# Kernel optimization log

Hardware: AMD Instinct MI355X
Metric: run time of the kernel (lower is better)

## Reference

```python
import jax, jax.numpy as jnp
import numpy as np

N = 50000      # nodes
E = 800000     # edges (avg degree 16)
D = 64         # node_feature_dim
ED = 1         # edge_feature_dim
H = 128        # hidden_dim
G = 128        # graphs in batch
L = 3          # n_conv
EPS = 1e-5     # batchnorm eps


def setup_inputs() -> dict:
    key = jax.random.key(0)
    ks = jax.random.split(key, 20)
    w = lambda k, shp: (jax.random.normal(k, shp, dtype=jnp.float32)
                        / np.float32(np.sqrt(shp[-2] if len(shp) > 1 else 1.0)))
    return {
        "atom_z": jax.random.randint(ks[0], (N,), 0, 100),
        "edge_index": jax.random.randint(ks[1], (2, E), 0, N),
        "edge_attr": jax.random.normal(ks[2], (E, ED), dtype=jnp.float32),
        "batch": jnp.sort(jax.random.randint(ks[3], (N,), 0, G)),
        "emb": jax.random.normal(ks[4], (100, D), dtype=jnp.float32),
        "edge_W1": w(ks[5], (L, 2 * D + ED, H)), "edge_b1": jnp.zeros((L, H)),
        "edge_W2": w(ks[6], (L, H, H)),          "edge_b2": jnp.zeros((L, H)),
        "node_W1": w(ks[7], (L, D + H, H)),      "node_b1": jnp.zeros((L, H)),
        "node_W2": w(ks[8], (L, H, D)),          "node_b2": jnp.zeros((L, D)),
        "bn_gamma": jnp.ones((L, D)),            "bn_beta": jnp.zeros((L, D)),
        "out_W1": w(ks[9], (D, H)),  "out_b1": jnp.zeros((H,)),
        "out_W2": w(ks[10], (H, 1)), "out_b2": jnp.zeros((1,)),
    }


def reference(atom_z, edge_index, edge_attr, batch, emb,
              edge_W1, edge_b1, edge_W2, edge_b2,
              node_W1, node_b1, node_W2, node_b2,
              bn_gamma, bn_beta, out_W1, out_b1, out_W2, out_b2):
    sp = jax.nn.softplus
    src, dst = edge_index[0], edge_index[1]  # PyG source_to_target: x_j = x[src], x_i = x[dst]
    x = emb[atom_z]                          # [N, D]
    for l in range(L):
        # --- CGConv layer l ---
        z = jnp.concatenate([x[dst], x[src], edge_attr], axis=-1)        # [E, 2D+ED]
        m = sp(sp(z @ edge_W1[l] + edge_b1[l]) @ edge_W2[l] + edge_b2[l])  # [E, H]
        aggr = jax.ops.segment_sum(m, dst, num_segments=N)               # [N, H]
        h = jnp.concatenate([x, aggr], axis=-1)                          # [N, D+H]
        x = sp(h @ node_W1[l] + node_b1[l]) @ node_W2[l] + node_b2[l] + x
        # --- BatchNorm1d (training-mode batch stats) ---
        mu = jnp.mean(x, axis=0)
        var = jnp.mean(jnp.square(x - mu), axis=0)
        x = bn_gamma[l] * (x - mu) * jax.lax.rsqrt(var + EPS) + bn_beta[l]
    # --- global mean pool over graphs ---
    sums = jax.ops.segment_sum(x, batch, num_segments=G)                 # [G, D]
    cnts = jax.ops.segment_sum(jnp.ones((N, 1), x.dtype), batch, num_segments=G)
    pooled = sums / jnp.maximum(cnts, 1.0)
    # --- output MLP (dropout is identity at eval) ---
    out = sp(pooled @ out_W1 + out_b1) @ out_W2 + out_b2                 # [G, 1]
    return out
```

## Files before the change

kernel.cpp:

```cpp
#include <hip/hip_runtime.h>
#include <hip/hip_bf16.h>

#define N_NODES 50000
#define N_EDGES 800000
#define DIM 64
#define HID 128
#define NGRAPH 128
#define BN_EPS 1e-5f

typedef __attribute__((ext_vector_type(8))) short short8;
typedef __attribute__((ext_vector_type(4))) short short4v;
typedef __attribute__((ext_vector_type(4))) float f32x4;
typedef __attribute__((ext_vector_type(4))) int int4v;

__device__ __forceinline__ float sp_(float v) {
    return fmaxf(v, 0.f) + __logf(1.f + __expf(-fabsf(v)));
}
__device__ __forceinline__ short bfb(float f) {
    __hip_bfloat16 h = __float2bfloat16(f);
    return __builtin_bit_cast(short, h);
}
__device__ __forceinline__ float b2f(short s) {
    unsigned u = ((unsigned)(unsigned short)s) << 16;
    return __builtin_bit_cast(float, u);
}

__global__ void k_embed(const int* __restrict__ az, const float* __restrict__ emb,
                        float* __restrict__ x, __hip_bfloat16* __restrict__ xb) {
    int idx = blockIdx.x * 256 + threadIdx.x;
    if (idx >= N_NODES * DIM) return;
    int n = idx >> 6;
    int d = idx & 63;
    float v = emb[az[n] * DIM + d];
    x[idx] = v;
    xb[idx] = __float2bfloat16(v);
}

__global__ void k_wprep(const float* __restrict__ src, short* __restrict__ dst,
                        int total, int nshift, int srcStride) {
    int l = blockIdx.y;
    int idx = blockIdx.x * 256 + threadIdx.x;
    if (idx >= total) return;
    int K = total >> nshift;
    int k = idx >> nshift;
    int n = idx & ((1 << nshift) - 1);
    dst[(size_t)l * total + n * K + k] = bfb(src[(size_t)l * srcStride + idx]);
}

__global__ void k_hist(const int* __restrict__ edst, int* __restrict__ deg) {
    int e = blockIdx.x * 256 + threadIdx.x;
    if (e < N_EDGES) atomicAdd(&deg[edst[e]], 1);
}

__global__ void k_scan(const int* __restrict__ deg, int* __restrict__ cursor) {
    __shared__ int wsum[16];
    __shared__ int carry;
    const int t = threadIdx.x, lane = t & 63, w = t >> 6;
    if (t == 0) carry = 0;
    __syncthreads();
    for (int base = 0; base < N_NODES; base += 1024) {
        int i = base + t;
        int v = (i < N_NODES) ? deg[i] : 0;
        int s = v;
#pragma unroll
        for (int off = 1; off < 64; off <<= 1) {
            int u = __shfl_up(s, off);
            if (lane >= off) s += u;
        }
        if (lane == 63) wsum[w] = s;
        __syncthreads();
        if (w == 0) {
            int ws = (lane < 16) ? wsum[lane] : 0;
#pragma unroll
            for (int off = 1; off < 16; off <<= 1) {
                int u = __shfl_up(ws, off);
                if (lane >= off) ws += u;
            }
            if (lane < 16) wsum[lane] = ws;
        }
        __syncthreads();
        int woff = (w == 0) ? 0 : wsum[w - 1];
        int excl = carry + woff + s - v;
        if (i < N_NODES) cursor[i] = excl;
        __syncthreads();
        if (t == 1023) carry += wsum[15];
        __syncthreads();
    }
}

__global__ void k_scatter(const int* __restrict__ esrc, const int* __restrict__ edst,
                          const float* __restrict__ eattr, int* __restrict__ cursor,
                          int* __restrict__ ssrc, int* __restrict__ sdst,
                          float* __restrict__ sattr) {
    int e = blockIdx.x * 256 + threadIdx.x;
    if (e >= N_EDGES) return;
    int d = edst[e];
    int pos = atomicAdd(&cursor[d], 1);
    ssrc[pos] = esrc[e];
    sdst[pos] = d;
    sattr[pos] = eattr[e];
}

__global__ void k_gbounds(const int* __restrict__ batch, int* __restrict__ gstart) {
    int g = threadIdx.x;
    if (g > NGRAPH) return;
    int lo = 0, hi = N_NODES;
    while (lo < hi) {
        int mid = (lo + hi) >> 1;
        if (batch[mid] < g) lo = mid + 1; else hi = mid;
    }
    gstart[g] = lo;
}

__launch_bounds__(512, 4)
__global__ void k_edge(const __hip_bfloat16* __restrict__ xb,
                       const int* __restrict__ ssrc, const int* __restrict__ sdst,
                       const float* __restrict__ sattr,
                       const float* __restrict__ W1f, const float* __restrict__ b1,
                       const float* __restrict__ b2,
                       const short* __restrict__ w1T, const short* __restrict__ w2T,
                       float* __restrict__ aggr) {
    __shared__ short zt[64 * 128];
    __shared__ short ht[64 * 128];
    __shared__ float attr_s[64];
    __shared__ int   dst_s[64];
    __shared__ int   seg_start[65];
    __shared__ int   seg_dst[64];
    __shared__ int   nseg_s;

    const int t = threadIdx.x;
    const int wid = t >> 6, lane = t & 63;
    const int lrow = lane & 15, lk = lane >> 4;
    const int r = t >> 3, q = t & 7;
    const int col = wid * 16 + lrow;

    short8 w1f[4], w2f[4];
#pragma unroll
    for (int ks = 0; ks < 4; ks++) {
        int kb = ks * 64 + lk * 16;
        w1f[ks] = *(const short8*)((const char*)w1T + col * 256 + kb);
        w2f[ks] = *(const short8*)((const char*)w2T + col * 256 + kb);
    }
    const float b1v = b1[col];
    const float b2v = b2[col];
    const float wlv = W1f[128 * 128 + col];

    const int NT = N_EDGES / 64;
    const int tile0 = blockIdx.x * 25;
    const int tile1 = (tile0 + 25 < NT) ? tile0 + 25 : NT;

    for (int tile = tile0; tile < tile1; ++tile) {
        const int e0 = tile * 64;
        {
            int e = e0 + r;
            int dn = sdst[e], sn = ssrc[e];
            if (q == 0) { dst_s[r] = dn; attr_s[r] = sattr[e]; }
            int node = (q < 4) ? dn : sn;
            const __hip_bfloat16* xr = xb + (size_t)node * DIM + (q & 3) * 16;
            int4v v0 = *(const int4v*)(xr);
            int4v v1 = *(const int4v*)(xr + 8);
            int cb = (q >> 2) * 128 + (q & 3) * 32;
            *(int4v*)((char*)zt + r * 256 + (cb ^ ((r & 7) << 4))) = v0;
            *(int4v*)((char*)zt + r * 256 + ((cb + 16) ^ ((r & 7) << 4))) = v1;
        }
        __syncthreads();

        if (wid == 0) {
            int d = dst_s[lane];
            int prev = (lane == 0) ? -1 : dst_s[lane - 1];
            bool start = (d != prev);
            unsigned long long mask = __ballot(start);
            int sidx = __popcll(mask & ((1ull << lane) - 1));
            if (start) { seg_start[sidx] = lane; seg_dst[sidx] = d; }
            if (lane == 63) {
                int ns = __popcll(mask);
                nseg_s = ns;
                seg_start[ns] = 64;
            }
        }

        f32x4 acc[4];
#pragma unroll
        for (int mi = 0; mi < 4; mi++) acc[mi] = (f32x4){0.f, 0.f, 0.f, 0.f};
#pragma unroll
        for (int ks = 0; ks < 4; ks++) {
            int kb = ks * 64 + lk * 16;
            short8 av[4];
#pragma unroll
            for (int mi = 0; mi < 4; mi++) {
                int row = mi * 16 + lrow;
                av[mi] = *(const short8*)((const char*)zt + row * 256 + (kb ^ ((row & 7) << 4)));
            }
#pragma unroll
            for (int mi = 0; mi < 4; mi++)
                acc[mi] = __builtin_amdgcn_mfma_f32_16x16x32_bf16(av[mi], w1f[ks], acc[mi], 0, 0, 0);
        }
#pragma unroll
        for (int mi = 0; mi < 4; mi++) {
#pragma unroll
            for (int rr = 0; rr < 4; rr++) {
                int row = mi * 16 + lk * 4 + rr;
                float val = acc[mi][rr] + b1v + attr_s[row] * wlv;
                *(short*)((char*)ht + row * 256 + ((col * 2) ^ ((row & 7) << 4))) = bfb(sp_(val));
            }
        }
        __syncthreads();

        f32x4 acc2[4];
#pragma unroll
        for (int mi = 0; mi < 4; mi++) acc2[mi] = (f32x4){0.f, 0.f, 0.f, 0.f};
#pragma unroll
        for (int ks = 0; ks < 4; ks++) {
            int kb = ks * 64 + lk * 16;
            short8 av[4];
#pragma unroll
            for (int mi = 0; mi < 4; mi++) {
                int row = mi * 16 + lrow;
                av[mi] = *(const short8*)((const char*)ht + row * 256 + (kb ^ ((row & 7) << 4)));
            }
#pragma unroll
            for (int mi = 0; mi < 4; mi++)
                acc2[mi] = __builtin_amdgcn_mfma_f32_16x16x32_bf16(av[mi], w2f[ks], acc2[mi], 0, 0, 0);
        }
#pragma unroll
        for (int mi = 0; mi < 4; mi++) {
#pragma unroll
            for (int rr = 0; rr < 4; rr++) {
                int row = mi * 16 + lk * 4 + rr;
                float val = sp_(acc2[mi][rr] + b2v);
                *(short*)((char*)zt + row * 256 + ((col * 2) ^ ((row & 7) << 4))) = bfb(val);
            }
        }
        __syncthreads();

        {
            int nseg = nseg_s;
            int rcol = t & 127, h = t >> 7;
            for (int s = h; s < nseg; s += 4) {
                int r0 = seg_start[s], r1 = seg_start[s + 1];
                float sum = 0.f;
                for (int rr = r0; rr < r1; rr++)
                    sum += b2f(*(const short*)((const char*)zt + rr * 256 + ((rcol * 2) ^ ((rr & 7) << 4))));
                atomicAdd(&aggr[(size_t)seg_dst[s] * HID + rcol], sum);
            }
        }
        __syncthreads();
    }
}

__launch_bounds__(256, 3)
__global__ void k_node(const __hip_bfloat16* __restrict__ xb,
                       const float* __restrict__ xf,
                       const float* __restrict__ aggr,
                       const short* __restrict__ w1T, const float* __restrict__ b1,
                       const short* __restrict__ w2T, const float* __restrict__ b2,
                       float* __restrict__ y, float* __restrict__ stats) {
    __shared__ short at[64 * 192];
    __shared__ short ht[64 * 128];

    const int t = threadIdx.x;
    const int wid = t >> 6, lane = t & 63, lrow = lane & 15, lk = lane >> 4;
    const int n0 = blockIdx.x * 64;

    const int nc0 = wid * 32;
    short8 w1f[6][2];
    float b1v[2];
#pragma unroll
    for (int ni = 0; ni < 2; ni++) {
        int col = nc0 + ni * 16 + lrow;
#pragma unroll
        for (int ks = 0; ks < 6; ks++) {
            int kb = ks * 64 + lk * 16;
            w1f[ks][ni] = *(const short8*)((const char*)w1T + col * 384 + kb);
        }
        b1v[ni] = b1[col];
    }
    const int nc2 = wid * 16;
    const int col2 = nc2 + lrow;
    short8 w2f[4];
#pragma unroll
    for (int ks = 0; ks < 4; ks++)
        w2f[ks] = *(const short8*)((const char*)w2T + col2 * 256 + ks * 64 + lk * 16);
    const float b2v = b2[col2];

    if (t < 64) {
        int node = n0 + t;
        if (node < N_NODES) {
            const __hip_bfloat16* xr = xb + (size_t)node * DIM;
#pragma unroll
            for (int i = 0; i < 8; i++) {
                int4v v = *(const int4v*)(xr + i * 8);
                *(int4v*)((char*)at + t * 384 + ((i * 16) ^ ((t & 7) << 4))) = v;
            }
        } else {
            int4v z = {0, 0, 0, 0};
#pragma unroll
            for (int i = 0; i < 8; i++)
                *(int4v*)((char*)at + t * 384 + ((i * 16) ^ ((t & 7) << 4))) = z;
        }
    }
    {
        int r = t >> 2, q = t & 3;
        int node = n0 + r;
#pragma unroll
        for (int i = 0; i < 4; i++) {
            short8 s = {0, 0, 0, 0, 0, 0, 0, 0};
            if (node < N_NODES) {
                const float* ar = aggr + (size_t)node * HID + q * 32 + i * 8;
                float4 f0 = *(const float4*)ar;
                float4 f1 = *(const float4*)(ar + 4);
                s = (short8){bfb(f0.x), bfb(f0.y), bfb(f0.z), bfb(f0.w),
                             bfb(f1.x), bfb(f1.y), bfb(f1.z), bfb(f1.w)};
            }
            int cb = 128 + q * 64 + i * 16;
            *(short8*)((char*)at + r * 384 + (cb ^ ((r & 7) << 4))) = s;
        }
    }
    __syncthreads();

    f32x4 acc[4][2];
#pragma unroll
    for (int mi = 0; mi < 4; mi++)
#pragma unroll
        for (int ni = 0; ni < 2; ni++) acc[mi][ni] = (f32x4){0.f, 0.f, 0.f, 0.f};
#pragma unroll
    for (int ks = 0; ks < 6; ks++) {
        int kb = ks * 64 + lk * 16;
        short8 av[4];
#pragma unroll
        for (int mi = 0; mi < 4; mi++) {
            int row = mi * 16 + lrow;
            av[mi] = *(const short8*)((const char*)at + row * 384 + (kb ^ ((row & 7) << 4)));
        }
#pragma unroll
        for (int mi = 0; mi < 4; mi++)
#pragma unroll
            for (int ni = 0; ni < 2; ni++)
                acc[mi][ni] = __builtin_amdgcn_mfma_f32_16x16x32_bf16(av[mi], w1f[ks][ni], acc[mi][ni], 0, 0, 0);
    }
#pragma unroll
    for (int mi = 0; mi < 4; mi++) {
#pragma unroll
        for (int ni = 0; ni < 2; ni++) {
            int col = nc0 + ni * 16 + lrow;
#pragma unroll
            for (int rr = 0; rr < 4; rr++) {
                int row = mi * 16 + lk * 4 + rr;
                float val = sp_(acc[mi][ni][rr] + b1v[ni]);
                *(short*)((char*)ht + row * 256 + ((col * 2) ^ ((row & 7) << 4))) = bfb(val);
            }
        }
    }
    __syncthreads();

    f32x4 acc2[4];
#pragma unroll
    for (int mi = 0; mi < 4; mi++) acc2[mi] = (f32x4){0.f, 0.f, 0.f, 0.f};
#pragma unroll
    for (int ks = 0; ks < 4; ks++) {
        int kb = ks * 64 + lk * 16;
        short8 av[4];
#pragma unroll
        for (int mi = 0; mi < 4; mi++) {
            int row = mi * 16 + lrow;
            av[mi] = *(const short8*)((const char*)ht + row * 256 + (kb ^ ((row & 7) << 4)));
        }
#pragma unroll
        for (int mi = 0; mi < 4; mi++)
            acc2[mi] = __builtin_amdgcn_mfma_f32_16x16x32_bf16(av[mi], w2f[ks], acc2[mi], 0, 0, 0);
    }
    float s1 = 0.f, s2 = 0.f;
#pragma unroll
    for (int mi = 0; mi < 4; mi++) {
#pragma unroll
        for (int rr = 0; rr < 4; rr++) {
            int row = mi * 16 + lk * 4 + rr;
            int node = n0 + row;
            if (node < N_NODES) {
                float v = acc2[mi][rr] + b2v + xf[(size_t)node * DIM + col2];
                y[(size_t)node * DIM + col2] = v;
                s1 += v;
                s2 += v * v;
            }
        }
    }
    s1 += __shfl_xor(s1, 16); s1 += __shfl_xor(s1, 32);
    s2 += __shfl_xor(s2, 16); s2 += __shfl_xor(s2, 32);
    if (lane < 16) {
        atomicAdd(&stats[col2], s1);
        atomicAdd(&stats[64 + col2], s2);
    }
}

__global__ void k_bnfin(const float* __restrict__ gamma, const float* __restrict__ beta,
                        float* __restrict__ stats) {
    int d = threadIdx.x;
    float mu = stats[d] * (1.f / N_NODES);
    float var = stats[64 + d] * (1.f / N_NODES) - mu * mu;
    float rstd = rsqrtf(var + BN_EPS);
    float a = gamma[d] * rstd;
    stats[128 + d] = a;
    stats[192 + d] = beta[d] - mu * a;
}

__global__ void k_bnapply(const float* __restrict__ y, const float* __restrict__ stats,
                          float* __restrict__ x, __hip_bfloat16* __restrict__ xb) {
    int idx = (blockIdx.x * 256 + threadIdx.x) * 4;
    if (idx >= N_NODES * DIM) return;
    int d = idx & 63;
    float4 v = *(const float4*)(y + idx);
    float4 r;
    r.x = stats[128 + d + 0] * v.x + stats[192 + d + 0];
    r.y = stats[128 + d + 1] * v.y + stats[192 + d + 1];
    r.z = stats[128 + d + 2] * v.z + stats[192 + d + 2];
    r.w = stats[128 + d + 3] * v.w + stats[192 + d + 3];
    *(float4*)(x + idx) = r;
    short4v s = {bfb(r.x), bfb(r.y), bfb(r.z), bfb(r.w)};
    *(short4v*)((char*)(xb + idx)) = s;
}

__global__ void k_pool2(const int* __restrict__ gstart, const float* __restrict__ x,
                        float* __restrict__ pooled) {
    __shared__ float red[256];
    const int g = blockIdx.x, t = threadIdx.x;
    const int d = t & 63, nl = t >> 6;
    const int s = gstart[g], e = gstart[g + 1];
    float sum = 0.f;
    for (int n = s + nl; n < e; n += 4)
        sum += x[(size_t)n * DIM + d];
    red[t] = sum;
    __syncthreads();
    if (t < 64) {
        float tot = red[t] + red[t + 64] + red[t + 128] + red[t + 192];
        int c = e - s;
        pooled[g * DIM + t] = tot / fmaxf((float)c, 1.f);
    }
}

__global__ void k_out(const float* __restrict__ pooled,
                      const float* __restrict__ W1, const float* __restrict__ b1,
                      const float* __restrict__ W2, const float* __restrict__ b2,
                      float* __restrict__ out) {
    __shared__ float pl[64];
    __shared__ float wsum[2];
    int g = blockIdx.x, t = threadIdx.x;
    if (t < 64) pl[t] = pooled[g * 64 + t];
    __syncthreads();
    float a = b1[t];
#pragma unroll
    for (int d = 0; d < 64; d++) a += pl[d] * W1[d * 128 + t];
    float c = sp_(a) * W2[t];
#pragma unroll
    for (int off = 32; off >= 1; off >>= 1) c += __shfl_down(c, off);
    int lane = t & 63, wid = t >> 6;
    if (lane == 0) wsum[wid] = c;
    __syncthreads();
    if (t == 0) out[g] = wsum[0] + wsum[1] + b2[0];
}

extern "C" void kernel_launch(void* const* d_in, const int* in_sizes, int n_in,
                              void* d_out, int out_size, void* d_ws, size_t ws_size,
                              hipStream_t stream) {
    const int*   az    = (const int*)d_in[0];
    const int*   ei    = (const int*)d_in[1];
    const float* eattr = (const float*)d_in[2];
    const int*   batch = (const int*)d_in[3];
    const float* emb   = (const float*)d_in[4];
    const float* eW1   = (const float*)d_in[5];
    const float* eb1   = (const float*)d_in[6];
    const float* eW2   = (const float*)d_in[7];
    const float* eb2   = (const float*)d_in[8];
    const float* nW1   = (const float*)d_in[9];
    const float* nb1   = (const float*)d_in[10];
    const float* nW2   = (const float*)d_in[11];
    const float* nb2   = (const float*)d_in[12];
    const float* gam   = (const float*)d_in[13];
    const float* bet   = (const float*)d_in[14];
    const float* oW1   = (const float*)d_in[15];
    const float* ob1   = (const float*)d_in[16];
    const float* oW2   = (const float*)d_in[17];
    const float* ob2   = (const float*)d_in[18];
    const int* esrc = ei;
    const int* edst = ei + N_EDGES;

    float* x     = (float*)d_ws;
    float* y     = x + (size_t)N_NODES * DIM;
    float* aggr  = y + (size_t)N_NODES * DIM;
    float* stats = aggr + (size_t)N_NODES * HID;
    float* pooled = stats + 256;
    __hip_bfloat16* xb = (__hip_bfloat16*)(pooled + NGRAPH * DIM);
    short* ew1T = (short*)(xb + (size_t)N_NODES * DIM);
    short* ew2T = ew1T + 3 * 128 * 128;
    short* nw1T = ew2T + 3 * 128 * 128;
    short* nw2T = nw1T + 3 * 128 * 192;
    int*   cursor = (int*)(nw2T + 3 * 64 * 128);
    int*   ssrc   = cursor + N_NODES;
    int*   sdstA  = ssrc + N_EDGES;
    float* sattr  = (float*)(sdstA + N_EDGES);
    int*   gstart = (int*)(sattr + N_EDGES);

    k_embed<<<(N_NODES * DIM + 255) / 256, 256, 0, stream>>>(az, emb, x, xb);

    k_wprep<<<dim3(64, 3), 256, 0, stream>>>(eW1, ew1T, 128 * 128, 7, 129 * 128);
    k_wprep<<<dim3(64, 3), 256, 0, stream>>>(eW2, ew2T, 128 * 128, 7, 128 * 128);
    k_wprep<<<dim3(96, 3), 256, 0, stream>>>(nW1, nw1T, 192 * 128, 7, 192 * 128);
    k_wprep<<<dim3(32, 3), 256, 0, stream>>>(nW2, nw2T, 128 * 64, 6, 128 * 64);

    hipMemsetAsync(cursor, 0, N_NODES * sizeof(int), stream);
    k_hist<<<(N_EDGES + 255) / 256, 256, 0, stream>>>(edst, cursor);
    k_scan<<<1, 1024, 0, stream>>>(cursor, cursor);
    k_scatter<<<(N_EDGES + 255) / 256, 256, 0, stream>>>(esrc, edst, eattr, cursor,
                                                         ssrc, sdstA, sattr);
    k_gbounds<<<1, 256, 0, stream>>>(batch, gstart);

    for (int l = 0; l < 3; l++) {
        hipMemsetAsync(aggr, 0, ((size_t)N_NODES * HID + 256) * sizeof(float), stream);
        k_edge<<<500, 512, 0, stream>>>(xb, ssrc, sdstA, sattr,
                                        eW1 + (size_t)l * 129 * 128, eb1 + l * 128, eb2 + l * 128,
                                        ew1T + (size_t)l * 128 * 128, ew2T + (size_t)l * 128 * 128,
                                        aggr);
        k_node<<<(N_NODES + 63) / 64, 256, 0, stream>>>(xb, x, aggr,
                                                        nw1T + (size_t)l * 128 * 192, nb1 + l * 128,
                                                        nw2T + (size_t)l * 64 * 128, nb2 + l * 64,
                                                        y, stats);
        k_bnfin<<<1, 64, 0, stream>>>(gam + l * 64, bet + l * 64, stats);
        k_bnapply<<<(N_NODES * DIM / 4 + 255) / 256, 256, 0, stream>>>(y, stats, x, xb);
    }

    k_pool2<<<NGRAPH, 256, 0, stream>>>(gstart, x, pooled);
    k_out<<<NGRAPH, 128, 0, stream>>>(pooled, oW1, ob1, oW2, ob2, (float*)d_out);
}
```

Measured before the change: 1.037 ms.

## Precompute per-node first-layer edge projections and gather them instead of raw features

The first edge-MLP matmul is split algebraically: x[dst]@W1a + x[src]@W1b is computed once per node in a new k_ab kernel, which writes a 128+128 bf16 projection per node. The edge kernel then gathers the two projections, adds them plus the edge-attribute term, and applies softplus, so one MFMA GEMM per edge tile is dropped. The message tile is also kept in fp32 in shared memory for the segment reduction. In exchange each edge gathers 512 bytes instead of 256, uses more LDS per block, and rounds the pre-activation sum to bf16.

```diff
diff --git a/kernel.cpp b/kernel.cpp
--- a/kernel.cpp
+++ b/kernel.cpp
@@ -112,17 +112,85 @@
     gstart[g] = lo;
 }
 
+__launch_bounds__(512, 2)
+__global__ void k_ab(const __hip_bfloat16* __restrict__ xb,
+                     const short* __restrict__ w1T, const float* __restrict__ b1,
+                     short* __restrict__ xab) {
+    __shared__ short xt[64 * 64];
+    __shared__ short ot[64 * 256];
+    const int t = threadIdx.x;
+    const int wid = t >> 6, lane = t & 63, lrow = lane & 15, lk = lane >> 4;
+    const int col = wid * 16 + lrow;
+    const int n0 = blockIdx.x * 64;
+
+    short8 wa[2], wb[2];
+#pragma unroll
+    for (int ks = 0; ks < 2; ks++) {
+        wa[ks] = *(const short8*)((const char*)w1T + col * 256 + ks * 64 + lk * 16);
+        wb[ks] = *(const short8*)((const char*)w1T + col * 256 + 128 + ks * 64 + lk * 16);
+    }
+    const float b1v = b1[col];
+
+    {
+        int r = t >> 3, q = t & 7;
+        int node = n0 + r;
+        int4v v = {0, 0, 0, 0};
+        if (node < N_NODES) v = *(const int4v*)(xb + (size_t)node * DIM + q * 8);
+        *(int4v*)((char*)xt + r * 128 + ((q * 16) ^ ((r & 7) << 4))) = v;
+    }
+    __syncthreads();
+
+    f32x4 aa[4], ab[4];
+#pragma unroll
+    for (int mi = 0; mi < 4; mi++) { aa[mi] = (f32x4){0.f,0.f,0.f,0.f}; ab[mi] = (f32x4){0.f,0.f,0.f,0.f}; }
+#pragma unroll
+    for (int ks = 0; ks < 2; ks++) {
+        int kb = ks * 64 + lk * 16;
+        short8 av[4];
+#pragma unroll
+        for (int mi = 0; mi < 4; mi++) {
+            int row = mi * 16 + lrow;
+            av[mi] = *(const short8*)((const char*)xt + row * 128 + (kb ^ ((row & 7) << 4)));
+        }
+#pragma unroll
+        for (int mi = 0; mi < 4; mi++) {
+            aa[mi] = __builtin_amdgcn_mfma_f32_16x16x32_bf16(av[mi], wa[ks], aa[mi], 0, 0, 0);
+            ab[mi] = __builtin_amdgcn_mfma_f32_16x16x32_bf16(av[mi], wb[ks], ab[mi], 0, 0, 0);
+        }
+    }
+#pragma unroll
+    for (int mi = 0; mi < 4; mi++) {
+#pragma unroll
+        for (int rr = 0; rr < 4; rr++) {
+            int row = mi * 16 + lk * 4 + rr;
+            int swz = (row & 7) << 4;
+            *(short*)((char*)ot + row * 512 + ((col * 2) ^ swz)) = bfb(aa[mi][rr] + b1v);
+            *(short*)((char*)ot + row * 512 + 256 + ((col * 2) ^ swz)) = bfb(ab[mi][rr]);
+        }
+    }
+    __syncthreads();
+#pragma unroll
+    for (int it = 0; it < 4; it++) {
+        int idx = it * 8192 + t * 16;
+        int row = idx >> 9, off = idx & 511;
+        int node = n0 + row;
+        if (node < N_NODES) {
+            int base = off & 256, lo = off & 255;
+            int4v v = *(const int4v*)((char*)ot + row * 512 + base + (lo ^ ((row & 7) << 4)));
+            *(int4v*)((char*)xab + (size_t)node * 512 + off) = v;
+        }
+    }
+}
+
 __launch_bounds__(512, 4)
-__global__ void k_edge(const __hip_bfloat16* __restrict__ xb,
+__global__ void k_edge(const short* __restrict__ xab,
                        const int* __restrict__ ssrc, const int* __restrict__ sdst,
                        const float* __restrict__ sattr,
-                       const float* __restrict__ W1f, const float* __restrict__ b1,
-                       const float* __restrict__ b2,
-                       const short* __restrict__ w1T, const short* __restrict__ w2T,
+                       const float* __restrict__ wl, const float* __restrict__ b2,
+                       const short* __restrict__ w2T,
                        float* __restrict__ aggr) {
-    __shared__ short zt[64 * 128];
     __shared__ short ht[64 * 128];
-    __shared__ float attr_s[64];
+    __shared__ float mt[64 * 128];
     __shared__ int   dst_s[64];
     __shared__ int   seg_start[65];
     __shared__ int   seg_dst[64];
@@ -134,16 +202,14 @@
     const int r = t >> 3, q = t & 7;
     const int col = wid * 16 + lrow;
 
-    short8 w1f[4], w2f[4];
-#pragma unroll
-    for (int ks = 0; ks < 4; ks++) {
-        int kb = ks * 64 + lk * 16;
-        w1f[ks] = *(const short8*)((const char*)w1T + col * 256 + kb);
-        w2f[ks] = *(const short8*)((const char*)w2T + col * 256 + kb);
-    }
-    const float b1v = b1[col];
+    short8 w2f[4];
+#pragma unroll
+    for (int ks = 0; ks < 4; ks++)
+        w2f[ks] = *(const short8*)((const char*)w2T + col * 256 + ks * 64 + lk * 16);
     const float b2v = b2[col];
-    const float wlv = W1f[128 * 128 + col];
+    float wlv[16];
+#pragma unroll
+    for (int i = 0; i < 16; i++) wlv[i] = wl[q * 16 + i];
 
     const int NT = N_EDGES / 64;
     const int tile0 = blockIdx.x * 25;
@@ -154,14 +220,21 @@
         {
             int e = e0 + r;
             int dn = sdst[e], sn = ssrc[e];
-            if (q == 0) { dst_s[r] = dn; attr_s[r] = sattr[e]; }
-            int node = (q < 4) ? dn : sn;
-            const __hip_bfloat16* xr = xb + (size_t)node * DIM + (q & 3) * 16;
-            int4v v0 = *(const int4v*)(xr);
-            int4v v1 = *(const int4v*)(xr + 8);
-            int cb = (q >> 2) * 128 + (q & 3) * 32;
-            *(int4v*)((char*)zt + r * 256 + (cb ^ ((r & 7) << 4))) = v0;
-            *(int4v*)((char*)zt + r * 256 + ((cb + 16) ^ ((r & 7) << 4))) = v1;
+            float at = sattr[e];
+            if (q == 0) dst_s[r] = dn;
+            const char* pa = (const char*)xab + (size_t)dn * 512 + q * 32;
+            const char* pb = (const char*)xab + (size_t)sn * 512 + 256 + q * 32;
+            short8 a0 = *(const short8*)pa, a1 = *(const short8*)(pa + 16);
+            short8 b0 = *(const short8*)pb, b1x = *(const short8*)(pb + 16);
+            short8 h0, h1;
+#pragma unroll
+            for (int i = 0; i < 8; i++) {
+                h0[i] = bfb(sp_(b2f(a0[i]) + b2f(b0[i]) + at * wlv[i]));
+                h1[i] = bfb(sp_(b2f(a1[i]) + b2f(b1x[i]) + at * wlv[8 + i]));
+            }
+            int swz = (r & 7) << 4;
+            *(short8*)((char*)ht + r * 256 + ((q * 32) ^ swz)) = h0;
+            *(short8*)((char*)ht + r * 256 + (((q * 32) + 16) ^ swz)) = h1;
         }
         __syncthreads();
 
@@ -179,9 +252,9 @@
             }
         }
 
-        f32x4 acc[4];
-#pragma unroll
-        for (int mi = 0; mi < 4; mi++) acc[mi] = (f32x4){0.f, 0.f, 0.f, 0.f};
+        f32x4 acc2[4];
+#pragma unroll
+        for (int mi = 0; mi < 4; mi++) acc2[mi] = (f32x4){0.f, 0.f, 0.f, 0.f};
 #pragma unroll
         for (int ks = 0; ks < 4; ks++) {
             int kb = ks * 64 + lk * 16;
@@ -189,46 +262,18 @@
 #pragma unroll
             for (int mi = 0; mi < 4; mi++) {
                 int row = mi * 16 + lrow;
-                av[mi] = *(const short8*)((const char*)zt + row * 256 + (kb ^ ((row & 7) << 4)));
+                av[mi] = *(const short8*)((const char*)ht + row * 256 + (kb ^ ((row & 7) << 4)));
             }
 #pragma unroll
             for (int mi = 0; mi < 4; mi++)
-                acc[mi] = __builtin_amdgcn_mfma_f32_16x16x32_bf16(av[mi], w1f[ks], acc[mi], 0, 0, 0);
+                acc2[mi] = __builtin_amdgcn_mfma_f32_16x16x32_bf16(av[mi], w2f[ks], acc2[mi], 0, 0, 0);
         }
 #pragma unroll
         for (int mi = 0; mi < 4; mi++) {
 #pragma unroll
             for (int rr = 0; rr < 4; rr++) {
                 int row = mi * 16 + lk * 4 + rr;
-                float val = acc[mi][rr] + b1v + attr_s[row] * wlv;
-                *(short*)((char*)ht + row * 256 + ((col * 2) ^ ((row & 7) << 4))) = bfb(sp_(val));
-            }
-        }
-        __syncthreads();
-
-        f32x4 acc2[4];
-#pragma unroll
-        for (int mi = 0; mi < 4; mi++) acc2[mi] = (f32x4){0.f, 0.f, 0.f, 0.f};
-#pragma unroll
-        for (int ks = 0; ks < 4; ks++) {
-            int kb = ks * 64 + lk * 16;
-            short8 av[4];
-#pragma unroll
-            for (int mi = 0; mi < 4; mi++) {
-                int row = mi * 16 + lrow;
-                av[mi] = *(const short8*)((const char*)ht + row * 256 + (kb ^ ((row & 7) << 4)));
-            }
-#pragma unroll
-            for (int mi = 0; mi < 4; mi++)
-                acc2[mi] = __builtin_amdgcn_mfma_f32_16x16x32_bf16(av[mi], w2f[ks], acc2[mi], 0, 0, 0);
-        }
-#pragma unroll
-        for (int mi = 0; mi < 4; mi++) {
-#pragma unroll
-            for (int rr = 0; rr < 4; rr++) {
-                int row = mi * 16 + lk * 4 + rr;
-                float val = sp_(acc2[mi][rr] + b2v);
-                *(short*)((char*)zt + row * 256 + ((col * 2) ^ ((row & 7) << 4))) = bfb(val);
+                *(float*)((char*)mt + row * 512 + ((col * 4) ^ ((row & 7) << 4))) = sp_(acc2[mi][rr] + b2v);
             }
         }
         __syncthreads();
@@ -240,7 +285,7 @@
                 int r0 = seg_start[s], r1 = seg_start[s + 1];
                 float sum = 0.f;
                 for (int rr = r0; rr < r1; rr++)
-                    sum += b2f(*(const short*)((const char*)zt + rr * 256 + ((rcol * 2) ^ ((rr & 7) << 4))));
+                    sum += *(const float*)((const char*)mt + rr * 512 + ((rcol * 4) ^ ((rr & 7) << 4)));
                 atomicAdd(&aggr[(size_t)seg_dst[s] * HID + rcol], sum);
             }
         }
@@ -498,6 +543,7 @@
     int*   sdstA  = ssrc + N_EDGES;
     float* sattr  = (float*)(sdstA + N_EDGES);
     int*   gstart = (int*)(sattr + N_EDGES);
+    short* xab    = (short*)(gstart + 256);
 
     k_embed<<<(N_NODES * DIM + 255) / 256, 256, 0, stream>>>(az, emb, x, xb);
 
@@ -515,9 +561,12 @@
 
     for (int l = 0; l < 3; l++) {
         hipMemsetAsync(aggr, 0, ((size_t)N_NODES * HID + 256) * sizeof(float), stream);
-        k_edge<<<500, 512, 0, stream>>>(xb, ssrc, sdstA, sattr,
-                                        eW1 + (size_t)l * 129 * 128, eb1 + l * 128, eb2 + l * 128,
-                                        ew1T + (size_t)l * 128 * 128, ew2T + (size_t)l * 128 * 128,
+        k_ab<<<(N_NODES + 63) / 64, 512, 0, stream>>>(xb, ew1T + (size_t)l * 128 * 128,
+                                                      eb1 + l * 128, xab);
+        k_edge<<<500, 512, 0, stream>>>(xab, ssrc, sdstA, sattr,
+                                        eW1 + (size_t)l * 129 * 128 + 128 * 128,
+                                        eb2 + l * 128,
+                                        ew2T + (size_t)l * 128 * 128,
                                         aggr);
         k_node<<<(N_NODES + 63) / 64, 256, 0, stream>>>(xb, x, aggr,
                                                         nw1T + (size_t)l * 128 * 192, nb1 + l * 128,
```

New measurement: 977.5 us. 1.06x faster.
